# Optimization experiments

Measured on AMD Instinct MI355X. Metric: run time of the kernel, lower is better.

The kernel has to match this reference:

```python
import jax, jax.numpy as jnp
import numpy as np

B, S, H = 16, 8192, 256

def setup_inputs() -> dict:
    key = jax.random.key(0)
    k1, k2, k3, k4, k5 = jax.random.split(key, 5)
    scale = 1.0 / np.sqrt(H)
    return {
        "hidden": jax.random.normal(k1, (B, H), dtype=jnp.float32),
        "encoder_outputs": jax.random.normal(k2, (B, S, H), dtype=jnp.float32),
        "W1": jax.random.uniform(k3, (H, H), dtype=jnp.float32, minval=-scale, maxval=scale),
        "W2": jax.random.uniform(k4, (H, H), dtype=jnp.float32, minval=-scale, maxval=scale),
        "V": jax.random.uniform(k5, (1, H), dtype=jnp.float32, minval=-scale, maxval=scale),
    }

def reference(hidden, encoder_outputs, W1, W2, V):
    # hidden: [B, H], encoder_outputs: [B, S, H]
    h1 = jnp.einsum('bh,kh->bk', hidden, W1)[:, None, :]        # [B, 1, H]
    h2 = jnp.einsum('bsh,kh->bsk', encoder_outputs, W2)          # [B, S, H]
    scores = jnp.einsum('bsh,oh->bso', jnp.tanh(h1 + h2), V)     # [B, S, 1]
    attn = jax.nn.softmax(scores, axis=1)                        # softmax over seq dim
    context = jnp.sum(attn * encoder_outputs, axis=1)            # [B, H]
    # torch: unsqueeze/transpose/repeat/squeeze/permute -> tile context over seq: [B, H, S]
    context_tiled = jnp.broadcast_to(context[:, :, None], (context.shape[0], context.shape[1], encoder_outputs.shape[1]))
    return (context_tiled, context, attn[:, :, 0])
```

## Files before the change

kernel.cpp:

```cpp
#include <hip/hip_runtime.h>
#include <hip/hip_bf16.h>
#include <math.h>

#define B_ 16
#define S_ 8192
#define H_ 256
#define NBLK 32
#define TILE_R 32
#define T_PER_BLK 8
#define LROW 264

using bf16x8 = __attribute__((ext_vector_type(8))) short;
using f32x4 = __attribute__((ext_vector_type(4))) float;

__device__ inline short f2bf(float x) {
  union {
    float f;
    unsigned u;
  } v;
  v.f = x;
  unsigned r = v.u + 0x7FFFu + ((v.u >> 16) & 1u);
  return (short)(r >> 16);
}

__device__ inline bf16x8 pack8(float4 a, float4 b) {
  union {
    __hip_bfloat162 h[4];
    bf16x8 v;
  } u;
  u.h[0] = __float22bfloat162_rn(make_float2(a.x, a.y));
  u.h[1] = __float22bfloat162_rn(make_float2(a.z, a.w));
  u.h[2] = __float22bfloat162_rn(make_float2(b.x, b.y));
  u.h[3] = __float22bfloat162_rn(make_float2(b.z, b.w));
  return u.v;
}

__device__ inline float fast_tanh(float x) {
  float e = exp2f(x * 2.885390082f);
  return fmaf(-2.f, __builtin_amdgcn_rcpf(e + 1.f), 1.f);
}

__global__ __launch_bounds__(256) void prep_kernel(
    const float* __restrict__ hidden, const float* __restrict__ W1,
    const float* __restrict__ W2, short* __restrict__ W2f,
    float* __restrict__ h1) {
  const int blk = blockIdx.x;
  const int t = threadIdx.x;
  if (blk < 32) {
    const int gid = blk * 256 + t;
    const int l = gid & 63;
    const int j0 = (gid >> 6) & 15;
    const int ks = gid >> 10;
    const int row = j0 * 16 + (l & 15);
    const int col = ks * 32 + (l >> 4) * 8;
    const float* wp = W2 + row * H_ + col;
    bf16x8 out;
#pragma unroll
    for (int i = 0; i < 8; ++i) out[i] = f2bf(wp[i]);
    *(bf16x8*)(W2f + (size_t)gid * 8) = out;
  } else {
    const int b = blk - 32;
    const float* hrow = hidden + b * H_;
    const float* wrow = W1 + t * H_;
    float acc = 0.f;
#pragma unroll 8
    for (int h = 0; h < H_; ++h) acc += hrow[h] * wrow[h];
    h1[b * H_ + t] = acc;
  }
}

__global__ __launch_bounds__(512, 4) void scores_ctx_kernel(
    const float* __restrict__ enc, const short* __restrict__ W2f,
    const float* __restrict__ h1, const float* __restrict__ V,
    float* __restrict__ expsc, float* __restrict__ c_blk,
    float* __restrict__ l_blk) {
  __shared__ __align__(16) short albuf[2][TILE_R * LROW];
  __shared__ float pcomb[8][33];
  __shared__ float avec[TILE_R];
  __shared__ float2 clds2[4][129];
  __shared__ float lsum[8];

  const int tid = threadIdx.x;
  const int w = tid >> 6;
  const int l = tid & 63;
  const int lo = l & 15;
  const int hi = l >> 4;
  const int bid = blockIdx.x;
  const int b = bid >> 5;
  const int blk = bid & 31;
  const int s_base = blk * (TILE_R * T_PER_BLK);

  const bf16x8* bbase = (const bf16x8*)W2f;
  bf16x8 bfrag[8][2];
#pragma unroll
  for (int ks = 0; ks < 8; ++ks)
#pragma unroll
    for (int jj = 0; jj < 2; ++jj)
      bfrag[ks][jj] = bbase[(ks * 16 + (2 * w + jj)) * 64 + l];

  float h1v[2], Vv[2];
#pragma unroll
  for (int jj = 0; jj < 2; ++jj) {
    h1v[jj] = h1[b * H_ + (2 * w + jj) * 16 + lo];
    Vv[jj] = V[(2 * w + jj) * 16 + lo];
  }

  const int r0 = tid >> 5;
  const int kc0 = tid & 31;
  const float4* gsrc = (const float4*)(enc + (size_t)b * S_ * H_);

  const int rg = tid >> 7;
  const int cp = tid & 127;
  float c0 = 0.f, c1 = 0.f, l_part = 0.f;

  {
    size_t gi0 = ((size_t)(s_base + r0) * (H_ / 4)) + kc0 * 2;
    size_t gi1 = ((size_t)(s_base + r0 + 16) * (H_ / 4)) + kc0 * 2;
    float4 a0 = gsrc[gi0], a1 = gsrc[gi0 + 1];
    float4 b0 = gsrc[gi1], b1 = gsrc[gi1 + 1];
    *(bf16x8*)&albuf[0][r0 * LROW + kc0 * 8] = pack8(a0, a1);
    *(bf16x8*)&albuf[0][(r0 + 16) * LROW + kc0 * 8] = pack8(b0, b1);
  }
  __syncthreads();

  const int b0s = lo & 1;
  const int b1s = (lo >> 1) & 1;
  const int b2s = (lo >> 2) & 1;

  for (int t = 0; t < T_PER_BLK; ++t) {
    const int cur = t & 1;

    float4 na0, na1, nb0, nb1;
    if (t + 1 < T_PER_BLK) {
      size_t gi0 =
          ((size_t)(s_base + (t + 1) * TILE_R + r0) * (H_ / 4)) + kc0 * 2;
      size_t gi1 =
          ((size_t)(s_base + (t + 1) * TILE_R + r0 + 16) * (H_ / 4)) + kc0 * 2;
      na0 = gsrc[gi0];
      na1 = gsrc[gi0 + 1];
      nb0 = gsrc[gi1];
      nb1 = gsrc[gi1 + 1];
    }

    f32x4 acc[2][2];
#pragma unroll
    for (int m = 0; m < 2; ++m)
#pragma unroll
      for (int jj = 0; jj < 2; ++jj) acc[m][jj] = (f32x4){0.f, 0.f, 0.f, 0.f};

    const short* abase = &albuf[cur][lo * LROW + hi * 8];
#pragma unroll
    for (int ks = 0; ks < 8; ++ks) {
      bf16x8 a0 = *(const bf16x8*)(abase + ks * 32);
      bf16x8 a1 = *(const bf16x8*)(abase + 16 * LROW + ks * 32);
      acc[0][0] = __builtin_amdgcn_mfma_f32_16x16x32_bf16(a0, bfrag[ks][0], acc[0][0], 0, 0, 0);
      acc[0][1] = __builtin_amdgcn_mfma_f32_16x16x32_bf16(a0, bfrag[ks][1], acc[0][1], 0, 0, 0);
      acc[1][0] = __builtin_amdgcn_mfma_f32_16x16x32_bf16(a1, bfrag[ks][0], acc[1][0], 0, 0, 0);
      acc[1][1] = __builtin_amdgcn_mfma_f32_16x16x32_bf16(a1, bfrag[ks][1], acc[1][1], 0, 0, 0);
    }

    float p0 = fast_tanh(acc[0][0][0] + h1v[0]) * Vv[0] + fast_tanh(acc[0][1][0] + h1v[1]) * Vv[1];
    float p1 = fast_tanh(acc[0][0][1] + h1v[0]) * Vv[0] + fast_tanh(acc[0][1][1] + h1v[1]) * Vv[1];
    float p2 = fast_tanh(acc[0][0][2] + h1v[0]) * Vv[0] + fast_tanh(acc[0][1][2] + h1v[1]) * Vv[1];
    float p3 = fast_tanh(acc[0][0][3] + h1v[0]) * Vv[0] + fast_tanh(acc[0][1][3] + h1v[1]) * Vv[1];
    float p4 = fast_tanh(acc[1][0][0] + h1v[0]) * Vv[0] + fast_tanh(acc[1][1][0] + h1v[1]) * Vv[1];
    float p5 = fast_tanh(acc[1][0][1] + h1v[0]) * Vv[0] + fast_tanh(acc[1][1][1] + h1v[1]) * Vv[1];
    float p6 = fast_tanh(acc[1][0][2] + h1v[0]) * Vv[0] + fast_tanh(acc[1][1][2] + h1v[1]) * Vv[1];
    float p7 = fast_tanh(acc[1][0][3] + h1v[0]) * Vv[0] + fast_tanh(acc[1][1][3] + h1v[1]) * Vv[1];

    float q0 = (b0s ? p1 : p0) + __shfl_xor((b0s ? p0 : p1), 1, 16);
    float q1 = (b0s ? p3 : p2) + __shfl_xor((b0s ? p2 : p3), 1, 16);
    float q2 = (b0s ? p5 : p4) + __shfl_xor((b0s ? p4 : p5), 1, 16);
    float q3 = (b0s ? p7 : p6) + __shfl_xor((b0s ? p6 : p7), 1, 16);
    float r0q = (b1s ? q1 : q0) + __shfl_xor((b1s ? q0 : q1), 2, 16);
    float r1q = (b1s ? q3 : q2) + __shfl_xor((b1s ? q2 : q3), 2, 16);
    float u = (b2s ? r1q : r0q) + __shfl_xor((b2s ? r0q : r1q), 4, 16);
    u += __shfl_xor(u, 8, 16);

    if (lo < 8) {
      const int row = ((lo >> 2) & 1) * 16 + hi * 4 + (lo & 3);
      pcomb[w][row] = u;
    }
    __syncthreads();

    if (t + 1 < T_PER_BLK) {
      *(bf16x8*)&albuf[cur ^ 1][r0 * LROW + kc0 * 8] = pack8(na0, na1);
      *(bf16x8*)&albuf[cur ^ 1][(r0 + 16) * LROW + kc0 * 8] = pack8(nb0, nb1);
    }

    if (l < 4) {
      const int row = w * 4 + l;
      float s = 0.f;
#pragma unroll
      for (int ww = 0; ww < 8; ++ww) s += pcomb[ww][row];
      float e = exp2f(s * 1.44269504f);
      avec[row] = e;
      expsc[(size_t)b * S_ + s_base + t * TILE_R + row] = e;
      l_part += e;
    }
    __syncthreads();

    const unsigned* ab32 = (const unsigned*)&albuf[cur][0];
#pragma unroll
    for (int k = 0; k < 8; ++k) {
      const int r = rg * 8 + k;
      unsigned vb = ab32[r * 132 + cp];
      float a = avec[r];
      float he = __uint_as_float(vb << 16);
      float ho = __uint_as_float(vb & 0xFFFF0000u);
      c0 = fmaf(a, he, c0);
      c1 = fmaf(a, ho, c1);
    }
  }

  float lp = l_part;
  lp += __shfl_xor(lp, 1);
  lp += __shfl_xor(lp, 2);
  if (l == 0) lsum[w] = lp;
  clds2[rg][cp] = make_float2(c0, c1);
  __syncthreads();
  if (tid < 128) {
    float2 s0 = clds2[0][tid], s1 = clds2[1][tid];
    float2 s2 = clds2[2][tid], s3 = clds2[3][tid];
    float2 r;
    r.x = s0.x + s1.x + s2.x + s3.x;
    r.y = s0.y + s1.y + s2.y + s3.y;
    ((float2*)(c_blk + ((size_t)(b * NBLK + blk)) * H_))[tid] = r;
  }
  if (tid == 0) {
    float ls = 0.f;
#pragma unroll
    for (int ww = 0; ww < 8; ++ww) ls += lsum[ww];
    l_blk[b * NBLK + blk] = ls;
  }
}

__global__ __launch_bounds__(256) void finish_kernel(
    const float* __restrict__ expsc, const float* __restrict__ l_blk,
    const float* __restrict__ c_blk, float* __restrict__ out0,
    float* __restrict__ out1, float* __restrict__ out2) {
  const int bx = blockIdx.x;
  const int b = blockIdx.y;
  const int tid = threadIdx.x;
  float lg = 0.f;
#pragma unroll
  for (int j = 0; j < NBLK; ++j) lg += l_blk[b * NBLK + j];
  const float inv = 1.f / lg;

  if (bx < 4) {
    const size_t base = (size_t)b * S_ + bx * 2048;
    const float4* ip = (const float4*)(expsc + base);
    float4* op = (float4*)(out2 + base);
    float4 x0 = ip[tid * 2];
    float4 x1 = ip[tid * 2 + 1];
    float4 y0 = {x0.x * inv, x0.y * inv, x0.z * inv, x0.w * inv};
    float4 y1 = {x1.x * inv, x1.y * inv, x1.z * inv, x1.w * inv};
    op[tid * 2] = y0;
    op[tid * 2 + 1] = y1;
  } else {
    const int h = bx - 4;
    float cs = 0.f;
#pragma unroll
    for (int j = 0; j < NBLK; ++j)
      cs += c_blk[((size_t)(b * NBLK + j)) * H_ + h];
    const float ctx = cs * inv;
    if (tid == 0) out1[b * H_ + h] = ctx;
    float4 vv = {ctx, ctx, ctx, ctx};
    float4* op = (float4*)(out0 + ((size_t)b * H_ + h) * S_);
#pragma unroll 4
    for (int i = tid; i < S_ / 4; i += 256) op[i] = vv;
  }
}

extern "C" void kernel_launch(void* const* d_in, const int* in_sizes, int n_in,
                              void* d_out, int out_size, void* d_ws,
                              size_t ws_size, hipStream_t stream) {
  const float* hidden = (const float*)d_in[0];
  const float* enc = (const float*)d_in[1];
  const float* W1 = (const float*)d_in[2];
  const float* W2 = (const float*)d_in[3];
  const float* V = (const float*)d_in[4];

  float* out0 = (float*)d_out;
  float* out1 = out0 + (size_t)B_ * H_ * S_;
  float* out2 = out1 + B_ * H_;

  float* ws = (float*)d_ws;
  short* W2f = (short*)ws;
  float* h1 = ws + 32768;
  float* expsc = h1 + B_ * H_;
  float* l_blk = expsc + (size_t)B_ * S_;
  float* c_blk = l_blk + B_ * NBLK;

  prep_kernel<<<48, 256, 0, stream>>>(hidden, W1, W2, W2f, h1);
  scores_ctx_kernel<<<B_ * NBLK, 512, 0, stream>>>(enc, W2f, h1, V, expsc,
                                                   c_blk, l_blk);
  finish_kernel<<<dim3(H_ + 4, B_), 256, 0, stream>>>(expsc, l_blk, c_blk,
                                                      out0, out1, out2);
}
```

Before: 76.67 us.

## Software-pipeline context accumulation one tile behind to drop a barrier per tile

Grows the bf16 encoder tile buffer from two to four slots and double-buffers the partial-score and exp-weight arrays. The weighted context accumulation for tile t-1 now runs in iteration t, after the exp computation, so one __syncthreads per tile iteration goes away. A final barrier and epilogue handle the last tile. In exchange, LDS use roughly doubles (about 34KB to 68KB per block), which may lower occupancy under launch_bounds(512,4).

```diff
diff --git a/kernel.cpp b/kernel.cpp
--- a/kernel.cpp
+++ b/kernel.cpp
@@ -74,9 +74,9 @@
     const float* __restrict__ h1, const float* __restrict__ V,
     float* __restrict__ expsc, float* __restrict__ c_blk,
     float* __restrict__ l_blk) {
-  __shared__ __align__(16) short albuf[2][TILE_R * LROW];
-  __shared__ float pcomb[8][33];
-  __shared__ float avec[TILE_R];
+  __shared__ __align__(16) short albuf[4][TILE_R * LROW];
+  __shared__ float pcomb[2][8][33];
+  __shared__ float avec[2][TILE_R];
   __shared__ float2 clds2[4][129];
   __shared__ float lsum[8];
 
@@ -128,7 +128,8 @@
   const int b2s = (lo >> 2) & 1;
 
   for (int t = 0; t < T_PER_BLK; ++t) {
-    const int cur = t & 1;
+    const int cur = t & 3;
+    const int par = t & 1;
 
     float4 na0, na1, nb0, nb1;
     if (t + 1 < T_PER_BLK) {
@@ -179,33 +180,52 @@
 
     if (lo < 8) {
       const int row = ((lo >> 2) & 1) * 16 + hi * 4 + (lo & 3);
-      pcomb[w][row] = u;
+      pcomb[par][w][row] = u;
+    }
+
+    if (t + 1 < T_PER_BLK) {
+      *(bf16x8*)&albuf[(t + 1) & 3][r0 * LROW + kc0 * 8] = pack8(na0, na1);
+      *(bf16x8*)&albuf[(t + 1) & 3][(r0 + 16) * LROW + kc0 * 8] =
+          pack8(nb0, nb1);
     }
     __syncthreads();
-
-    if (t + 1 < T_PER_BLK) {
-      *(bf16x8*)&albuf[cur ^ 1][r0 * LROW + kc0 * 8] = pack8(na0, na1);
-      *(bf16x8*)&albuf[cur ^ 1][(r0 + 16) * LROW + kc0 * 8] = pack8(nb0, nb1);
-    }
 
     if (l < 4) {
       const int row = w * 4 + l;
       float s = 0.f;
 #pragma unroll
-      for (int ww = 0; ww < 8; ++ww) s += pcomb[ww][row];
+      for (int ww = 0; ww < 8; ++ww) s += pcomb[par][ww][row];
       float e = exp2f(s * 1.44269504f);
-      avec[row] = e;
+      avec[par][row] = e;
       expsc[(size_t)b * S_ + s_base + t * TILE_R + row] = e;
       l_part += e;
     }
-    __syncthreads();
-
-    const unsigned* ab32 = (const unsigned*)&albuf[cur][0];
+
+    if (t >= 1) {
+      const unsigned* ab32 = (const unsigned*)&albuf[(t - 1) & 3][0];
+      const float* av = avec[(t - 1) & 1];
+#pragma unroll
+      for (int k = 0; k < 8; ++k) {
+        const int r = rg * 8 + k;
+        unsigned vb = ab32[r * 132 + cp];
+        float a = av[r];
+        float he = __uint_as_float(vb << 16);
+        float ho = __uint_as_float(vb & 0xFFFF0000u);
+        c0 = fmaf(a, he, c0);
+        c1 = fmaf(a, ho, c1);
+      }
+    }
+  }
+
+  __syncthreads();
+  {
+    const unsigned* ab32 = (const unsigned*)&albuf[(T_PER_BLK - 1) & 3][0];
+    const float* av = avec[(T_PER_BLK - 1) & 1];
 #pragma unroll
     for (int k = 0; k < 8; ++k) {
       const int r = rg * 8 + k;
       unsigned vb = ab32[r * 132 + cp];
-      float a = avec[r];
+      float a = av[r];
       float he = __uint_as_float(vb << 16);
       float ho = __uint_as_float(vb & 0xFFFF0000u);
       c0 = fmaf(a, he, c0);
```

After: 80.57 us. 1.05x slower.
